# Performance work log

Measured on AMD Instinct MI355X. Metric: run time of the kernel, lower is better.

Reference implementation:

```python
import jax, jax.numpy as jnp
import numpy as np

B, LC, LP = 8, 1024, 512
D, H, F, V, NL = 512, 8, 2048, 70, 4
MAXLEN = 2048
HD = D // H
EPS = 1e-5


def setup_inputs() -> dict:
    key = jax.random.key(0)
    ks = iter(jax.random.split(key, 64))
    s = lambda *sh: jax.random.normal(next(ks), sh, jnp.float32) * 0.02
    inp = {}
    inp['cds'] = jax.random.randint(next(ks), (B, LC), 0, V)
    inp['enc_prot'] = jax.random.normal(next(ks), (B, LP, D), jnp.float32)
    causal = jnp.tril(jnp.ones((LC, LC), jnp.int32))
    inp['cds_mask'] = jnp.broadcast_to(causal[None, None], (B, 1, LC, LC))
    inp['prot_mask'] = jnp.ones((B, 1, 1, LP), jnp.int32)
    inp['tok_emb'] = s(V, D)
    inp['pos_emb'] = s(MAXLEN, D)
    for p in ['sa', 'ca']:
        for m in ['q', 'k', 'v', 'o']:
            inp[f'{p}_w{m}'] = s(NL, D, D)
            inp[f'{p}_b{m}'] = jnp.zeros((NL, D), jnp.float32)
    inp['ff_w1'] = s(NL, D, F)
    inp['ff_b1'] = jnp.zeros((NL, F), jnp.float32)
    inp['ff_w2'] = s(NL, F, D)
    inp['ff_b2'] = jnp.zeros((NL, D), jnp.float32)
    for i in [1, 2, 3]:
        inp[f'ln{i}_g'] = jnp.ones((NL, D), jnp.float32)
        inp[f'ln{i}_b'] = jnp.zeros((NL, D), jnp.float32)
    inp['fc_out_w'] = s(D, V)
    inp['fc_out_b'] = jnp.zeros((V,), jnp.float32)
    return inp


def layernorm(x, g, b):
    mu = jnp.mean(x, -1, keepdims=True)
    var = jnp.var(x, -1, keepdims=True)
    return (x - mu) * jax.lax.rsqrt(var + EPS) * g + b


def mha(q_in, k_in, v_in, wq, bq, wk, bk, wv, bv, wo, bo, mask):
    b, lq, _ = q_in.shape
    lk = k_in.shape[1]
    q = (q_in @ wq + bq).reshape(b, lq, H, HD).transpose(0, 2, 1, 3)
    k = (k_in @ wk + bk).reshape(b, lk, H, HD).transpose(0, 2, 1, 3)
    v = (v_in @ wv + bv).reshape(b, lk, H, HD).transpose(0, 2, 1, 3)
    scores = jnp.einsum('bhqd,bhkd->bhqk', q, k) / jnp.sqrt(jnp.float32(HD))
    scores = jnp.where(mask == 0, -jnp.inf, scores)
    attn = jax.nn.softmax(scores, axis=-1)
    out = jnp.einsum('bhqk,bhkd->bhqd', attn, v)
    out = out.transpose(0, 2, 1, 3).reshape(b, lq, D)
    return out @ wo + bo, attn


def reference(cds, enc_prot, cds_mask, prot_mask, tok_emb, pos_emb,
              sa_wq, sa_bq, sa_wk, sa_bk, sa_wv, sa_bv, sa_wo, sa_bo,
              ca_wq, ca_bq, ca_wk, ca_bk, ca_wv, ca_bv, ca_wo, ca_bo,
              ff_w1, ff_b1, ff_w2, ff_b2,
              ln1_g, ln1_b, ln2_g, ln2_b, ln3_g, ln3_b,
              fc_out_w, fc_out_b):
    lc = cds.shape[1]
    x = tok_emb[cds] * jnp.sqrt(jnp.float32(D)) + pos_emb[:lc][None]
    attn = None
    for i in range(NL):
        sa, _ = mha(x, x, x, sa_wq[i], sa_bq[i], sa_wk[i], sa_bk[i],
                    sa_wv[i], sa_bv[i], sa_wo[i], sa_bo[i], cds_mask)
        x = layernorm(x + sa, ln1_g[i], ln1_b[i])
        ca, attn = mha(x, enc_prot, enc_prot, ca_wq[i], ca_bq[i], ca_wk[i], ca_bk[i],
                       ca_wv[i], ca_bv[i], ca_wo[i], ca_bo[i], prot_mask)
        x = layernorm(x + ca, ln2_g[i], ln2_b[i])
        ff = jax.nn.relu(x @ ff_w1[i] + ff_b1[i]) @ ff_w2[i] + ff_b2[i]
        x = layernorm(x + ff, ln3_g[i], ln3_b[i])
    logits = x @ fc_out_w + fc_out_b
    return logits, attn
```

## Files before the change

kernel.cpp:

```cpp
#include <hip/hip_runtime.h>

typedef __attribute__((ext_vector_type(8))) short bf16x8;
typedef __attribute__((ext_vector_type(4))) short bf16x4;
typedef __attribute__((ext_vector_type(2))) short bf16x2;
typedef __attribute__((ext_vector_type(4))) float f32x4;

#define D_MODEL 512
#define N_HEADS 8
#define HEAD_DIM 64
#define SEQ_C 1024
#define SEQ_P 512
#define BATCH 8
#define FFDIM 2048
#define VOCAB 70
#define NLAYER 4
#define MQ (BATCH*SEQ_C)
#define MKV (BATCH*SEQ_P)
#define KSTR 72
#define SCALE2 0.18033688011112043f

__device__ __forceinline__ short f2bs(float f) {
  union { float f; unsigned u; } v; v.f = f;
  unsigned r = (v.u + 0x7FFFu + ((v.u >> 16) & 1u)) >> 16;
  return (short)r;
}

__device__ __forceinline__ float bs2f(short s) {
  union { float f; unsigned u; } v;
  v.u = ((unsigned)(unsigned short)s) << 16;
  return v.f;
}

__device__ __forceinline__ void gl_lds16(const void* g, void* l) {
  __builtin_amdgcn_global_load_lds(
      (const __attribute__((address_space(1))) void*)g,
      (__attribute__((address_space(3))) void*)l, 16, 0, 0);
}

__global__ __launch_bounds__(256)
void embed_kernel(const int* __restrict__ cds, const float* __restrict__ tok,
                  const float* __restrict__ pos, short* __restrict__ xb) {
  int idx = (blockIdx.x * 256 + threadIdx.x) * 4;
  int row = idx >> 9, c = idx & 511;
  int l = row & (SEQ_C - 1);
  int t = cds[row];
  float4 tv = *(const float4*)(tok + (size_t)t * D_MODEL + c);
  float4 pv = *(const float4*)(pos + (size_t)l * D_MODEL + c);
  bf16x4 o;
  o[0] = f2bs(tv.x * 22.627416997969522f + pv.x);
  o[1] = f2bs(tv.y * 22.627416997969522f + pv.y);
  o[2] = f2bs(tv.z * 22.627416997969522f + pv.z);
  o[3] = f2bs(tv.w * 22.627416997969522f + pv.w);
  *(bf16x4*)(xb + idx) = o;
}

__global__ __launch_bounds__(256)
void cvtf2b_kernel(const float* __restrict__ in, short* __restrict__ out) {
  int i = (blockIdx.x * 256 + threadIdx.x) * 4;
  float4 v = *(const float4*)(in + i);
  bf16x4 o;
  o[0] = f2bs(v.x); o[1] = f2bs(v.y); o[2] = f2bs(v.z); o[3] = f2bs(v.w);
  *(bf16x4*)(out + i) = o;
}

struct WtArgs {
  const float* src[8];
  short* dst[8];
  size_t ldz[8];
  int row_off[8];
};

__global__ __launch_bounds__(256)
void wtrans8_kernel(WtArgs a) {
  __shared__ float T[32][33];
  int z = blockIdx.z;
  int job = z >> 2, layer = z & 3;
  const float* W = a.src[job] + (size_t)layer * D_MODEL * D_MODEL;
  short* Wt = a.dst[job] + (size_t)layer * a.ldz[job];
  int row_off = a.row_off[job];
  int n0 = blockIdx.x * 32, k0 = blockIdx.y * 32;
  int r = threadIdx.x >> 3, c4 = (threadIdx.x & 7) * 4;
  float4 v = *(const float4*)(W + (size_t)(k0 + r) * D_MODEL + n0 + c4);
  T[c4 + 0][r] = v.x; T[c4 + 1][r] = v.y; T[c4 + 2][r] = v.z; T[c4 + 3][r] = v.w;
  __syncthreads();
  bf16x4 o;
  o[0] = f2bs(T[r][c4 + 0]); o[1] = f2bs(T[r][c4 + 1]);
  o[2] = f2bs(T[r][c4 + 2]); o[3] = f2bs(T[r][c4 + 3]);
  *(bf16x4*)&Wt[(size_t)(row_off + n0 + r) * D_MODEL + k0 + c4] = o;
}

__global__ __launch_bounds__(256)
void wtrans_kernel(const float* __restrict__ W, short* __restrict__ Wt,
                   int K, int N, size_t dst_ldz) {
  __shared__ float T[32][33];
  size_t lo_s = (size_t)blockIdx.z * K * N;
  size_t lo_d = (size_t)blockIdx.z * dst_ldz;
  int n0 = blockIdx.x * 32, k0 = blockIdx.y * 32;
  int r = threadIdx.x >> 3, c4 = (threadIdx.x & 7) * 4;
  float4 v = *(const float4*)(W + lo_s + (size_t)(k0 + r) * N + n0 + c4);
  T[c4 + 0][r] = v.x; T[c4 + 1][r] = v.y; T[c4 + 2][r] = v.z; T[c4 + 3][r] = v.w;
  __syncthreads();
  bf16x4 o;
  o[0] = f2bs(T[r][c4 + 0]); o[1] = f2bs(T[r][c4 + 1]);
  o[2] = f2bs(T[r][c4 + 2]); o[3] = f2bs(T[r][c4 + 3]);
  *(bf16x4*)&Wt[lo_d + (size_t)(n0 + r) * K + k0 + c4] = o;
}

__global__ __launch_bounds__(256)
void logits_wt_kernel(const float* __restrict__ w, short* __restrict__ wt) {
  int idx = blockIdx.x * 256 + threadIdx.x;
  int r = idx >> 9, c = idx & 511;
  wt[idx] = (r < VOCAB) ? f2bs(w[c * VOCAB + r]) : (short)0;
}

template<int ACT, int OMODE, int MT, int KSPLIT = 0>
__global__ __launch_bounds__(256)
void gemm_mfma(const short* __restrict__ Ab, const short* __restrict__ Wt,
               const float* __restrict__ b0, const float* __restrict__ b1,
               const float* __restrict__ b2,
               float* __restrict__ Cf, float* __restrict__ Cf2,
               short* __restrict__ Cb,
               int N, int K, int ldc, size_t segstride) {
  constexpr int MREP = MT / 32;
  __shared__ __align__(16) short As[2][MT * 32];
  __shared__ __align__(16) short Bs[2][4096];
  int tid = threadIdx.x, lane = tid & 63, w = tid >> 6;
  int quad = lane >> 4, ln = lane & 15;
  int row0 = blockIdx.x * MT, col0 = blockIdx.y * 128;
  int kz = KSPLIT ? (int)blockIdx.z : 0;
  int Keff = KSPLIT ? (K >> 1) : K;
  int koff = kz * Keff;
  int q0 = tid, q1 = tid + 256;
  const short* a0 = Ab + (size_t)(row0 + (q0 >> 2)) * K + koff + (q0 & 3) * 8;
  const short* a1 = Ab + (size_t)(row0 + (q1 >> 2)) * K + koff + (q1 & 3) * 8;
  const short* w0 = Wt + (size_t)(col0 + (q0 >> 2)) * K + koff + (q0 & 3) * 8;
  const short* w1 = Wt + (size_t)(col0 + (q1 >> 2)) * K + koff + (q1 & 3) * 8;
  int wr = (w >> 1) * (MT / 2), wc = (w & 1) * 64;
  f32x4 acc[MREP][4];
  #pragma unroll
  for (int mb = 0; mb < MREP; mb++)
    #pragma unroll
    for (int nb = 0; nb < 4; nb++) acc[mb][nb] = (f32x4){0.f, 0.f, 0.f, 0.f};

  int nt = Keff >> 5;
#define STG(ko, buf) do { \
    gl_lds16(a0 + (ko), &As[buf][w * 512]); \
    if (MT == 128) gl_lds16(a1 + (ko), &As[buf][MT * 16 + w * 512]); \
    gl_lds16(w0 + (ko), &Bs[buf][w * 512]); \
    gl_lds16(w1 + (ko), &Bs[buf][2048 + w * 512]); } while (0)

  STG(0, 0);
  __syncthreads();
  for (int t = 0; t < nt; t++) {
    int cur = t & 1;
    if (t + 1 < nt) STG((t + 1) << 5, cur ^ 1);
    bf16x8 af[MREP], bfr[4];
    #pragma unroll
    for (int i = 0; i < MREP; i++)
      af[i] = *(const bf16x8*)&As[cur][(wr + i * 16 + ln) * 32 + quad * 8];
    #pragma unroll
    for (int i = 0; i < 4; i++)
      bfr[i] = *(const bf16x8*)&Bs[cur][(wc + i * 16 + ln) * 32 + quad * 8];
    #pragma unroll
    for (int mb = 0; mb < MREP; mb++)
      #pragma unroll
      for (int nb = 0; nb < 4; nb++)
        acc[mb][nb] = __builtin_amdgcn_mfma_f32_16x16x32_bf16(
            af[mb], bfr[nb], acc[mb][nb], 0, 0, 0);
    __syncthreads();
  }
#undef STG

  int colb = col0 + wc;
  const float* bp = b0;
  if (OMODE == 2) {
    int seg = colb >> 9;
    bp = (seg == 0) ? b0 : (seg == 1) ? b1 : b2;
  }
  float bv[4];
  #pragma unroll
  for (int nb = 0; nb < 4; nb++) {
    int col = colb + nb * 16 + ln;
    if (KSPLIT && kz)    bv[nb] = 0.f;
    else if (OMODE == 3) bv[nb] = (col < ldc) ? bp[col] : 0.f;
    else if (OMODE == 2) bv[nb] = bp[col & 511];
    else                 bv[nb] = bp[col];
  }
  float* Co = (KSPLIT && kz) ? Cf2 : Cf;
  size_t segoff = (OMODE == 2) ? (size_t)(colb >> 9) * segstride : 0;
  #pragma unroll
  for (int mb = 0; mb < MREP; mb++)
    #pragma unroll
    for (int i = 0; i < 4; i++) {
      size_t r = (size_t)(row0 + wr + mb * 16 + quad * 4 + i);
      #pragma unroll
      for (int nb = 0; nb < 4; nb++) {
        int col = colb + nb * 16 + ln;
        float v = acc[mb][nb][i] + bv[nb];
        if (ACT) v = fmaxf(v, 0.f);
        if (OMODE == 0)      Co[r * ldc + col] = v;
        else if (OMODE == 1) Cb[r * ldc + col] = f2bs(v);
        else if (OMODE == 2) Cb[segoff + r * 512 + (col & 511)] = f2bs(v);
        else if (col < ldc)  Co[r * ldc + col] = v;
      }
    }
}

__global__ __launch_bounds__(256)
void gemm_mega(const short* __restrict__ A0, const short* __restrict__ W0,
               const float* __restrict__ bq, const float* __restrict__ bk,
               const float* __restrict__ bv0, short* __restrict__ out0,
               const short* __restrict__ A1, const short* __restrict__ W1,
               const float* __restrict__ bk2, const float* __restrict__ bv2,
               short* __restrict__ out1) {
  __shared__ __align__(16) short As[2][4096];
  __shared__ __align__(16) short Bs[2][4096];
  const int K = 512;
  int bid = blockIdx.x;
  int job = bid >= 768;
  const short* Ab; const short* Wt; int row0, col0;
  if (!job) { Ab = A0; Wt = W0; row0 = (bid & 63) << 7; col0 = (bid >> 6) << 7; }
  else { int b2 = bid - 768; Ab = A1; Wt = W1; row0 = (b2 & 31) << 7; col0 = (b2 >> 5) << 7; }
  int tid = threadIdx.x, lane = tid & 63, w = tid >> 6;
  int quad = lane >> 4, ln = lane & 15;
  int q0 = tid, q1 = tid + 256;
  const short* a0 = Ab + (size_t)(row0 + (q0 >> 2)) * K + (q0 & 3) * 8;
  const short* a1 = Ab + (size_t)(row0 + (q1 >> 2)) * K + (q1 & 3) * 8;
  const short* w0 = Wt + (size_t)(col0 + (q0 >> 2)) * K + (q0 & 3) * 8;
  const short* w1 = Wt + (size_t)(col0 + (q1 >> 2)) * K + (q1 & 3) * 8;
  int wr = (w >> 1) * 64, wc = (w & 1) * 64;
  f32x4 acc[4][4];
  #pragma unroll
  for (int mb = 0; mb < 4; mb++)
    #pragma unroll
    for (int nb = 0; nb < 4; nb++) acc[mb][nb] = (f32x4){0.f, 0.f, 0.f, 0.f};

#define STG(ko, buf) do { \
    gl_lds16(a0 + (ko), &As[buf][w * 512]); \
    gl_lds16(a1 + (ko), &As[buf][2048 + w * 512]); \
    gl_lds16(w0 + (ko), &Bs[buf][w * 512]); \
    gl_lds16(w1 + (ko), &Bs[buf][2048 + w * 512]); } while (0)

  STG(0, 0);
  __syncthreads();
  for (int t = 0; t < 16; t++) {
    int cur = t & 1;
    if (t + 1 < 16) STG((t + 1) << 5, cur ^ 1);
    bf16x8 af[4], bfr[4];
    #pragma unroll
    for (int i = 0; i < 4; i++) {
      af[i]  = *(const bf16x8*)&As[cur][(wr + i * 16 + ln) * 32 + quad * 8];
      bfr[i] = *(const bf16x8*)&Bs[cur][(wc + i * 16 + ln) * 32 + quad * 8];
    }
    #pragma unroll
    for (int mb = 0; mb < 4; mb++)
      #pragma unroll
      for (int nb = 0; nb < 4; nb++)
        acc[mb][nb] = __builtin_amdgcn_mfma_f32_16x16x32_bf16(
            af[mb], bfr[nb], acc[mb][nb], 0, 0, 0);
    __syncthreads();
  }
#undef STG

  int colb = col0 + wc;
  int seg = colb >> 9;
  const float* bp = job ? (seg ? bv2 : bk2)
                        : (seg == 0 ? bq : seg == 1 ? bk : bv0);
  short* ob = job ? (out1 + (size_t)seg * ((size_t)MKV * D_MODEL))
                  : (out0 + (size_t)seg * ((size_t)MQ * D_MODEL));
  float bvv[4];
  #pragma unroll
  for (int nb = 0; nb < 4; nb++) bvv[nb] = bp[(colb + nb * 16 + ln) & 511];
  #pragma unroll
  for (int mb = 0; mb < 4; mb++)
    #pragma unroll
    for (int i = 0; i < 4; i++) {
      size_t r = (size_t)(row0 + wr + mb * 16 + quad * 4 + i);
      #pragma unroll
      for (int nb = 0; nb < 4; nb++) {
        int col = colb + nb * 16 + ln;
        ob[r * 512 + (col & 511)] = f2bs(acc[mb][nb][i] + bvv[nb]);
      }
    }
}

template<bool CAUSAL, bool SAVE_ML>
__global__ __launch_bounds__(512)
void flash_mfma(const short* __restrict__ Q, const short* __restrict__ K,
                const short* __restrict__ V, short* __restrict__ O,
                float* __restrict__ m_out, float* __restrict__ l_out,
                int LQ, int LK) {
  __shared__ short Ks[2][64 * KSTR];
  __shared__ short Vt[2][64 * KSTR];
  __shared__ short Ps[8 * 16 * KSTR];
  int qt = CAUSAL ? ((int)gridDim.x - 1 - (int)blockIdx.x) : (int)blockIdx.x;
  int bh = blockIdx.y;
  int b = bh >> 3, h = bh & 7;
  int tid = threadIdx.x, lane = tid & 63, w = tid >> 6;
  int quad = lane >> 4, ln = lane & 15;

  const short* qp = Q + (size_t)(b * LQ + qt * 128 + w * 16 + ln) * D_MODEL + h * HEAD_DIM;
  bf16x8 qf[2];
  qf[0] = *(const bf16x8*)(qp + quad * 8);
  qf[1] = *(const bf16x8*)(qp + 32 + quad * 8);

  int qrow = qt * 128 + w * 16 + ln;
  float m_q = -__builtin_inff(), l_q = 0.f;
  f32x4 o_acc[4];
  #pragma unroll
  for (int nb = 0; nb < 4; nb++) o_acc[nb] = (f32x4){0.f, 0.f, 0.f, 0.f};

  const short* Kb = K + (size_t)(b * LK) * D_MODEL + h * HEAD_DIM;
  const short* Vb = V + (size_t)(b * LK) * D_MODEL + h * HEAD_DIM;
  int sr = tid >> 3, sc = (tid & 7) * 8;
  int br4 = (tid >> 4) * 4, bc4 = (tid & 15) * 4;
  bool vst = tid < 256;

  bf16x8 kr;
  bf16x4 vr0, vr1, vr2, vr3;

#define LOADKV(KT) do { \
    kr = *(const bf16x8*)(Kb + (size_t)((KT) * 64 + sr) * D_MODEL + sc); \
    if (vst) { \
      const short* vg_ = Vb + (size_t)((KT) * 64 + br4) * D_MODEL + bc4; \
      vr0 = *(const bf16x4*)(vg_); \
      vr1 = *(const bf16x4*)(vg_ + D_MODEL); \
      vr2 = *(const bf16x4*)(vg_ + 2 * D_MODEL); \
      vr3 = *(const bf16x4*)(vg_ + 3 * D_MODEL); } } while (0)

#define STORKV(BUF) do { \
    *(bf16x8*)&Ks[BUF][sr * KSTR + sc] = kr; \
    if (vst) { \
      _Pragma("unroll") \
      for (int jj = 0; jj < 4; jj++) { \
        bf16x4 t_; \
        t_[0] = vr0[jj]; t_[1] = vr1[jj]; t_[2] = vr2[jj]; t_[3] = vr3[jj]; \
        *(bf16x4*)&Vt[BUF][(bc4 + jj) * KSTR + br4] = t_; } } } while (0)

  int nkt = CAUSAL ? (2 * qt + 2) : (LK >> 6);
  LOADKV(0);
  STORKV(0);
  if (nkt > 1) LOADKV(1);
  __syncthreads();

  for (int kt = 0; kt < nkt; kt++) {
    int cur = kt & 1;
    if (kt + 1 < nkt) {
      STORKV(cur ^ 1);
      if (kt + 2 < nkt) LOADKV(kt + 2);
    }

    f32x4 st[4];
    __builtin_amdgcn_s_setprio(1);
    #pragma unroll
    for (int nb = 0; nb < 4; nb++) {
      st[nb] = (f32x4){0.f, 0.f, 0.f, 0.f};
      bf16x8 kf0 = *(const bf16x8*)&Ks[cur][(nb * 16 + ln) * KSTR + quad * 8];
      bf16x8 kf1 = *(const bf16x8*)&Ks[cur][(nb * 16 + ln) * KSTR + 32 + quad * 8];
      st[nb] = __builtin_amdgcn_mfma_f32_16x16x32_bf16(kf0, qf[0], st[nb], 0, 0, 0);
      st[nb] = __builtin_amdgcn_mfma_f32_16x16x32_bf16(kf1, qf[1], st[nb], 0, 0, 0);
    }
    __builtin_amdgcn_s_setprio(0);

    float sv[4][4];
    float mt = -__builtin_inff();
    if (CAUSAL && (kt * 64 + 63 > qt * 128 + w * 16)) {
      #pragma unroll
      for (int nb = 0; nb < 4; nb++)
        #pragma unroll
        for (int i = 0; i < 4; i++) {
          float v = st[nb][i] * SCALE2;
          if ((kt * 64 + nb * 16 + quad * 4 + i) > qrow) v = -__builtin_inff();
          sv[nb][i] = v;
          mt = fmaxf(mt, v);
        }
    } else {
      #pragma unroll
      for (int nb = 0; nb < 4; nb++)
        #pragma unroll
        for (int i = 0; i < 4; i++) {
          float v = st[nb][i] * SCALE2;
          sv[nb][i] = v;
          mt = fmaxf(mt, v);
        }
    }
    mt = fmaxf(mt, __shfl_xor(mt, 16));
    mt = fmaxf(mt, __shfl_xor(mt, 32));
    bool skip = __all(mt <= m_q + 8.0f) != 0;
    float mnew = skip ? m_q : fmaxf(m_q, mt);
    if (!skip) {
      float alpha = __builtin_amdgcn_exp2f(m_q - mnew);
      l_q *= alpha;
      #pragma unroll
      for (int i = 0; i < 4; i++) {
        float ai = __shfl(alpha, ((lane >> 4) << 2) + i);
        #pragma unroll
        for (int nb = 0; nb < 4; nb++) o_acc[nb][i] *= ai;
      }
    }
    m_q = mnew;

    float rs = 0.f;
    unsigned pu[4][2];
    #pragma unroll
    for (int nb = 0; nb < 4; nb++) {
      float p0 = __builtin_amdgcn_exp2f(sv[nb][0] - mnew);
      float p1 = __builtin_amdgcn_exp2f(sv[nb][1] - mnew);
      float p2 = __builtin_amdgcn_exp2f(sv[nb][2] - mnew);
      float p3 = __builtin_amdgcn_exp2f(sv[nb][3] - mnew);
      rs += (p0 + p1) + (p2 + p3);
      asm("v_cvt_pk_bf16_f32 %0, %1, %2" : "=v"(pu[nb][0]) : "v"(p0), "v"(p1));
      asm("v_cvt_pk_bf16_f32 %0, %1, %2" : "=v"(pu[nb][1]) : "v"(p2), "v"(p3));
    }
    rs += __shfl_xor(rs, 16);
    rs += __shfl_xor(rs, 32);
    l_q += rs;

    #pragma unroll
    for (int nb = 0; nb < 4; nb++) {
      union { unsigned u[2]; bf16x4 v; } uu;
      uu.u[0] = pu[nb][0]; uu.u[1] = pu[nb][1];
      *(bf16x4*)&Ps[w * 16 * KSTR + ln * KSTR + nb * 16 + quad * 4] = uu.v;
    }

    __builtin_amdgcn_s_setprio(1);
    #pragma unroll
    for (int kb = 0; kb < 2; kb++) {
      bf16x8 pf = *(const bf16x8*)&Ps[w * 16 * KSTR + ln * KSTR + kb * 32 + quad * 8];
      #pragma unroll
      for (int nb = 0; nb < 4; nb++) {
        bf16x8 vf = *(const bf16x8*)&Vt[cur][(nb * 16 + ln) * KSTR + kb * 32 + quad * 8];
        o_acc[nb] = __builtin_amdgcn_mfma_f32_16x16x32_bf16(pf, vf, o_acc[nb], 0, 0, 0);
      }
    }
    __builtin_amdgcn_s_setprio(0);
    __syncthreads();
  }
#undef LOADKV
#undef STORKV

  short* Ob = O + (size_t)(b * LQ + qt * 128 + w * 16 + quad * 4) * D_MODEL + h * HEAD_DIM;
  #pragma unroll
  for (int i = 0; i < 4; i++) {
    float li = __shfl(l_q, ((lane >> 4) << 2) + i);
    float inv = 1.f / li;
    #pragma unroll
    for (int nb = 0; nb < 4; nb++)
      Ob[(size_t)i * D_MODEL + nb * 16 + ln] = f2bs(o_acc[nb][i] * inv);
  }
  if (SAVE_ML && lane < 16) {
    int r = bh * LQ + qt * 128 + w * 16 + lane;
    m_out[r] = m_q;
    l_out[r] = l_q;
  }
}

__global__ __launch_bounds__(256)
void attn_prob_mfma(const short* __restrict__ Q, const short* __restrict__ K,
                    const float* __restrict__ m_in, const float* __restrict__ l_in,
                    float* __restrict__ out) {
  __shared__ short Ks[64 * KSTR];
  int qt = blockIdx.x, bh = blockIdx.y;
  int b = bh >> 3, h = bh & 7;
  int tid = threadIdx.x, lane = tid & 63, w = tid >> 6;
  int quad = lane >> 4, ln = lane & 15;
  const short* qp = Q + (size_t)(b * SEQ_C + qt * 64 + w * 16 + ln) * D_MODEL + h * HEAD_DIM;
  bf16x8 qf[2];
  qf[0] = *(const bf16x8*)(qp + quad * 8);
  qf[1] = *(const bf16x8*)(qp + 32 + quad * 8);
  float m_r[4], il[4];
  #pragma unroll
  for (int i = 0; i < 4; i++) {
    int r = bh * SEQ_C + qt * 64 + w * 16 + quad * 4 + i;
    m_r[i] = m_in[r]; il[i] = 1.f / l_in[r];
  }
  const short* Kb = K + (size_t)(b * SEQ_P) * D_MODEL + h * HEAD_DIM;
  int sr = tid >> 2, sc = (tid & 3) * 16;
  bf16x8 krA, krB;
  {
    const short* kg = Kb + (size_t)sr * D_MODEL + sc;
    krA = *(const bf16x8*)kg; krB = *(const bf16x8*)(kg + 8);
  }
  for (int kt = 0; kt < (SEQ_P >> 6); kt++) {
    __syncthreads();
    *(bf16x8*)&Ks[sr * KSTR + sc]     = krA;
    *(bf16x8*)&Ks[sr * KSTR + sc + 8] = krB;
    if (kt + 1 < (SEQ_P >> 6)) {
      const short* kg = Kb + (size_t)((kt + 1) * 64 + sr) * D_MODEL + sc;
      krA = *(const bf16x8*)kg; krB = *(const bf16x8*)(kg + 8);
    }
    __syncthreads();
    #pragma unroll
    for (int nb = 0; nb < 4; nb++) {
      f32x4 s = (f32x4){0.f, 0.f, 0.f, 0.f};
      bf16x8 kf0 = *(const bf16x8*)&Ks[(nb * 16 + ln) * KSTR + quad * 8];
      bf16x8 kf1 = *(const bf16x8*)&Ks[(nb * 16 + ln) * KSTR + 32 + quad * 8];
      s = __builtin_amdgcn_mfma_f32_16x16x32_bf16(qf[0], kf0, s, 0, 0, 0);
      s = __builtin_amdgcn_mfma_f32_16x16x32_bf16(qf[1], kf1, s, 0, 0, 0);
      #pragma unroll
      for (int i = 0; i < 4; i++) {
        size_t off = ((size_t)bh * SEQ_C + qt * 64 + w * 16 + quad * 4 + i) * SEQ_P
                   + kt * 64 + nb * 16 + ln;
        out[off] = __builtin_amdgcn_exp2f(s[i] * SCALE2 - m_r[i]) * il[i];
      }
    }
  }
}

template<int MODE>
__global__ __launch_bounds__(256)
void add_ln_kernel(short* __restrict__ xb, const short* __restrict__ ybf,
                   const float* __restrict__ yf, const float* __restrict__ y2f,
                   const float* __restrict__ g, const float* __restrict__ b) {
  int row = blockIdx.x * 4 + (threadIdx.x >> 6);
  int lane = threadIdx.x & 63;
  int c0 = lane * 8;
  short* xr = xb + (size_t)row * D_MODEL;
  float v[8]; float s = 0.f, sq = 0.f;
  bf16x8 xv = *(const bf16x8*)(xr + c0);
  if (MODE == 0) {
    bf16x8 yv = *(const bf16x8*)(ybf + (size_t)row * D_MODEL + c0);
    #pragma unroll
    for (int i = 0; i < 8; i++) {
      float t = bs2f(xv[i]) + bs2f(yv[i]);
      v[i] = t; s += t; sq += t * t;
    }
  } else {
    const float* yr = yf + (size_t)row * D_MODEL + c0;
    const float* y2r = y2f + (size_t)row * D_MODEL + c0;
    float4 a0 = *(const float4*)(yr);
    float4 a1 = *(const float4*)(yr + 4);
    float4 c0v = *(const float4*)(y2r);
    float4 c1v = *(const float4*)(y2r + 4);
    float ya[8] = {a0.x + c0v.x, a0.y + c0v.y, a0.z + c0v.z, a0.w + c0v.w,
                   a1.x + c1v.x, a1.y + c1v.y, a1.z + c1v.z, a1.w + c1v.w};
    #pragma unroll
    for (int i = 0; i < 8; i++) {
      float t = bs2f(xv[i]) + ya[i];
      v[i] = t; s += t; sq += t * t;
    }
  }
  #pragma unroll
  for (int m = 1; m < 64; m <<= 1) { s += __shfl_xor(s, m); sq += __shfl_xor(sq, m); }
  float mu = s * (1.0f / 512.0f);
  float var = sq * (1.0f / 512.0f) - mu * mu;
  float rstd = rsqrtf(var + 1e-5f);
  float4 g0 = *(const float4*)(g + c0);
  float4 g1 = *(const float4*)(g + c0 + 4);
  float4 b0 = *(const float4*)(b + c0);
  float4 b1 = *(const float4*)(b + c0 + 4);
  float ga[8] = {g0.x, g0.y, g0.z, g0.w, g1.x, g1.y, g1.z, g1.w};
  float ba[8] = {b0.x, b0.y, b0.z, b0.w, b1.x, b1.y, b1.z, b1.w};
  bf16x8 o;
  #pragma unroll
  for (int i = 0; i < 8; i++)
    o[i] = f2bs((v[i] - mu) * rstd * ga[i] + ba[i]);
  *(bf16x8*)(xr + c0) = o;
}

extern "C" void kernel_launch(void* const* d_in, const int* in_sizes, int n_in,
                              void* d_out, int out_size, void* d_ws, size_t ws_size,
                              hipStream_t stream) {
  (void)in_sizes; (void)n_in; (void)out_size; (void)ws_size;
  const int*   cds      = (const int*)d_in[0];
  const float* enc_prot = (const float*)d_in[1];
  const float* tok_emb  = (const float*)d_in[4];
  const float* pos_emb  = (const float*)d_in[5];
  const float* sa_wq = (const float*)d_in[6];  const float* sa_bq = (const float*)d_in[7];
  const float* sa_wk = (const float*)d_in[8];  const float* sa_bk = (const float*)d_in[9];
  const float* sa_wv = (const float*)d_in[10]; const float* sa_bv = (const float*)d_in[11];
  const float* sa_wo = (const float*)d_in[12]; const float* sa_bo = (const float*)d_in[13];
  const float* ca_wq = (const float*)d_in[14]; const float* ca_bq = (const float*)d_in[15];
  const float* ca_wk = (const float*)d_in[16]; const float* ca_bk = (const float*)d_in[17];
  const float* ca_wv = (const float*)d_in[18]; const float* ca_bv = (const float*)d_in[19];
  const float* ca_wo = (const float*)d_in[20]; const float* ca_bo = (const float*)d_in[21];
  const float* ff_w1 = (const float*)d_in[22]; const float* ff_b1 = (const float*)d_in[23];
  const float* ff_w2 = (const float*)d_in[24]; const float* ff_b2 = (const float*)d_in[25];
  const float* ln1_g = (const float*)d_in[26]; const float* ln1_b = (const float*)d_in[27];
  const float* ln2_g = (const float*)d_in[28]; const float* ln2_b = (const float*)d_in[29];
  const float* ln3_g = (const float*)d_in[30]; const float* ln3_b = (const float*)d_in[31];
  const float* fcw   = (const float*)d_in[32]; const float* fcb   = (const float*)d_in[33];

  float* y    = (float*)d_ws;
  float* mbuf = y + (size_t)MQ * D_MODEL;
  float* lbuf = mbuf + (size_t)BATCH * N_HEADS * SEQ_C;
  short* xb   = (short*)(lbuf + (size_t)BATCH * N_HEADS * SEQ_C);
  short* yb   = xb + (size_t)MQ * D_MODEL;
  short* qb   = yb + (size_t)MQ * D_MODEL;
  short* kb   = qb + (size_t)MQ * D_MODEL;
  short* vb   = kb + (size_t)MQ * D_MODEL;
  short* ctxb = vb + (size_t)MQ * D_MODEL;
  short* hb   = qb;
  short* encb = ctxb + (size_t)MQ * D_MODEL;
  short* ckb  = encb + (size_t)MKV * D_MODEL;
  short* cvb  = ckb + (size_t)MKV * D_MODEL;
  short* wtb  = cvb + (size_t)MKV * D_MODEL;
  short* wts  = wtb + (size_t)128 * D_MODEL;
  const size_t WSZ = (size_t)NLAYER * D_MODEL * D_MODEL;
  short* w_saqkv = wts;
  short* w_sao   = w_saqkv + 3 * WSZ;
  short* w_caq   = w_sao + WSZ;
  short* w_cakv  = w_caq + WSZ;
  short* w_cao   = w_cakv + 2 * WSZ;
  short* w_ff1   = w_cao + WSZ;
  short* w_ff2   = w_ff1 + (size_t)NLAYER * D_MODEL * FFDIM;
  float* y2   = (float*)(w_ff2 + (size_t)NLAYER * D_MODEL * FFDIM);

  float* logits = (float*)d_out;
  float* attn   = logits + (size_t)MQ * VOCAB;

  const size_t L1536 = (size_t)1536 * 512, L1024 = (size_t)1024 * 512, L512 = (size_t)512 * 512;

  embed_kernel<<<MQ * D_MODEL / 1024, 256, 0, stream>>>(cds, tok_emb, pos_emb, xb);
  cvtf2b_kernel<<<(size_t)MKV * D_MODEL / 1024, 256, 0, stream>>>(enc_prot, encb);
  logits_wt_kernel<<<128 * D_MODEL / 256, 256, 0, stream>>>(fcw, wtb);
  {
    WtArgs a;
    a.src[0] = sa_wq; a.dst[0] = w_saqkv; a.ldz[0] = L1536; a.row_off[0] = 0;
    a.src[1] = sa_wk; a.dst[1] = w_saqkv; a.ldz[1] = L1536; a.row_off[1] = 512;
    a.src[2] = sa_wv; a.dst[2] = w_saqkv; a.ldz[2] = L1536; a.row_off[2] = 1024;
    a.src[3] = sa_wo; a.dst[3] = w_sao;   a.ldz[3] = L512;  a.row_off[3] = 0;
    a.src[4] = ca_wq; a.dst[4] = w_caq;   a.ldz[4] = L512;  a.row_off[4] = 0;
    a.src[5] = ca_wk; a.dst[5] = w_cakv;  a.ldz[5] = L1024; a.row_off[5] = 0;
    a.src[6] = ca_wv; a.dst[6] = w_cakv;  a.ldz[6] = L1024; a.row_off[6] = 512;
    a.src[7] = ca_wo; a.dst[7] = w_cao;   a.ldz[7] = L512;  a.row_off[7] = 0;
    wtrans8_kernel<<<dim3(16, 16, 8 * NLAYER), 256, 0, stream>>>(a);
  }
  wtrans_kernel<<<dim3(FFDIM / 32, D_MODEL / 32, NLAYER), 256, 0, stream>>>(
      ff_w1, w_ff1, D_MODEL, FFDIM, (size_t)FFDIM * 512);
  wtrans_kernel<<<dim3(D_MODEL / 32, FFDIM / 32, NLAYER), 256, 0, stream>>>(
      ff_w2, w_ff2, FFDIM, D_MODEL, (size_t)512 * FFDIM);

  dim3 gq64(MQ / 64, D_MODEL / 128);
  dim3 gf1(MQ / 128, FFDIM / 128);
  dim3 gff2(MQ / 128, D_MODEL / 128, 2);
  dim3 glg(MQ / 64, 1);
  dim3 ga(SEQ_C / 128, BATCH * N_HEADS);
  dim3 gap(SEQ_C / 64, BATCH * N_HEADS);

  for (int i = 0; i < NLAYER; i++) {
    size_t wo_ = (size_t)i * D_MODEL * D_MODEL, bo_ = (size_t)i * D_MODEL;
    size_t wf_ = (size_t)i * D_MODEL * FFDIM;
    gemm_mega<<<dim3(1024), 256, 0, stream>>>(
        xb, w_saqkv + (size_t)i * L1536, sa_bq + bo_, sa_bk + bo_, sa_bv + bo_, qb,
        encb, w_cakv + (size_t)i * L1024, ca_bk + bo_, ca_bv + bo_, ckb);
    flash_mfma<true,  false><<<ga, 512, 0, stream>>>(qb, kb, vb, ctxb, nullptr, nullptr, SEQ_C, SEQ_C);
    gemm_mfma<0,1,64><<<gq64, 256, 0, stream>>>(ctxb, w_sao + wo_,
        sa_bo + bo_, nullptr, nullptr, nullptr, nullptr, yb, 512, 512, 512, 0);
    add_ln_kernel<0><<<MQ / 4, 256, 0, stream>>>(xb, yb, nullptr, nullptr, ln1_g + bo_, ln1_b + bo_);
    gemm_mfma<0,1,64><<<gq64, 256, 0, stream>>>(xb, w_caq + wo_,
        ca_bq + bo_, nullptr, nullptr, nullptr, nullptr, qb, 512, 512, 512, 0);
    if (i == NLAYER - 1) {
      flash_mfma<false, true><<<ga, 512, 0, stream>>>(qb, ckb, cvb, ctxb, mbuf, lbuf, SEQ_C, SEQ_P);
      attn_prob_mfma<<<gap, 256, 0, stream>>>(qb, ckb, mbuf, lbuf, attn);
    } else {
      flash_mfma<false, false><<<ga, 512, 0, stream>>>(qb, ckb, cvb, ctxb, nullptr, nullptr, SEQ_C, SEQ_P);
    }
    gemm_mfma<0,1,64><<<gq64, 256, 0, stream>>>(ctxb, w_cao + wo_,
        ca_bo + bo_, nullptr, nullptr, nullptr, nullptr, yb, 512, 512, 512, 0);
    add_ln_kernel<0><<<MQ / 4, 256, 0, stream>>>(xb, yb, nullptr, nullptr, ln2_g + bo_, ln2_b + bo_);
    gemm_mfma<1,1,128><<<gf1, 256, 0, stream>>>(xb, w_ff1 + wf_,
        ff_b1 + (size_t)i * FFDIM, nullptr, nullptr, nullptr, nullptr, hb, FFDIM, 512, FFDIM, 0);
    gemm_mfma<0,0,128,1><<<gff2, 256, 0, stream>>>(hb, w_ff2 + wf_,
        ff_b2 + bo_, nullptr, nullptr, y, y2, nullptr, 512, FFDIM, 512, 0);
    add_ln_kernel<1><<<MQ / 4, 256, 0, stream>>>(xb, nullptr, y, y2, ln3_g + bo_, ln3_b + bo_);
  }
  gemm_mfma<0,3,64><<<glg, 256, 0, stream>>>(xb, wtb,
      fcb, nullptr, nullptr, logits, nullptr, nullptr, 128, 512, VOCAB, 0);
}
```

Measured before the change: 1.145 ms.

## Process two 16-row query tiles per wave in flash attention with 256 threads

The flash attention kernel now runs 4 waves of 256 threads per block instead of 8 waves, and each wave handles 32 query rows as two 16-row sub-tiles. Every K and V fragment read from LDS now feeds two MFMAs, which halves LDS fragment traffic per unit of compute. The softmax logic moves into a helper called once per sub-tile, and the K/V staging loads are redistributed across the smaller thread count. The cost is higher register pressure (two accumulator sets and two score sets) and fewer waves per block to hide latency.

```diff
diff --git a/kernel.cpp b/kernel.cpp
--- a/kernel.cpp
+++ b/kernel.cpp
@@ -284,58 +284,123 @@
     }
 }
 
+template<bool CAUSAL>
+__device__ __forceinline__ void softmax_step(
+    f32x4 st[4], float& m_q, float& l_q, f32x4 o_acc[4],
+    int qrow, bool maybe_masked, int kbase, int quad, int lane,
+    unsigned pu[4][2]) {
+  float sv[4][4];
+  float mt = -__builtin_inff();
+  if (CAUSAL && maybe_masked) {
+    #pragma unroll
+    for (int nb = 0; nb < 4; nb++)
+      #pragma unroll
+      for (int i = 0; i < 4; i++) {
+        float v = st[nb][i] * SCALE2;
+        if ((kbase + nb * 16 + quad * 4 + i) > qrow) v = -__builtin_inff();
+        sv[nb][i] = v;
+        mt = fmaxf(mt, v);
+      }
+  } else {
+    #pragma unroll
+    for (int nb = 0; nb < 4; nb++)
+      #pragma unroll
+      for (int i = 0; i < 4; i++) {
+        float v = st[nb][i] * SCALE2;
+        sv[nb][i] = v;
+        mt = fmaxf(mt, v);
+      }
+  }
+  mt = fmaxf(mt, __shfl_xor(mt, 16));
+  mt = fmaxf(mt, __shfl_xor(mt, 32));
+  bool skip = __all(mt <= m_q + 8.0f) != 0;
+  float mnew = skip ? m_q : fmaxf(m_q, mt);
+  if (!skip) {
+    float alpha = __builtin_amdgcn_exp2f(m_q - mnew);
+    l_q *= alpha;
+    #pragma unroll
+    for (int i = 0; i < 4; i++) {
+      float ai = __shfl(alpha, ((lane >> 4) << 2) + i);
+      #pragma unroll
+      for (int nb = 0; nb < 4; nb++) o_acc[nb][i] *= ai;
+    }
+  }
+  m_q = mnew;
+  float rs = 0.f;
+  #pragma unroll
+  for (int nb = 0; nb < 4; nb++) {
+    float p0 = __builtin_amdgcn_exp2f(sv[nb][0] - mnew);
+    float p1 = __builtin_amdgcn_exp2f(sv[nb][1] - mnew);
+    float p2 = __builtin_amdgcn_exp2f(sv[nb][2] - mnew);
+    float p3 = __builtin_amdgcn_exp2f(sv[nb][3] - mnew);
+    rs += (p0 + p1) + (p2 + p3);
+    asm("v_cvt_pk_bf16_f32 %0, %1, %2" : "=v"(pu[nb][0]) : "v"(p0), "v"(p1));
+    asm("v_cvt_pk_bf16_f32 %0, %1, %2" : "=v"(pu[nb][1]) : "v"(p2), "v"(p3));
+  }
+  rs += __shfl_xor(rs, 16);
+  rs += __shfl_xor(rs, 32);
+  l_q += rs;
+}
+
 template<bool CAUSAL, bool SAVE_ML>
-__global__ __launch_bounds__(512)
+__global__ __launch_bounds__(256)
 void flash_mfma(const short* __restrict__ Q, const short* __restrict__ K,
                 const short* __restrict__ V, short* __restrict__ O,
                 float* __restrict__ m_out, float* __restrict__ l_out,
                 int LQ, int LK) {
   __shared__ short Ks[2][64 * KSTR];
   __shared__ short Vt[2][64 * KSTR];
-  __shared__ short Ps[8 * 16 * KSTR];
+  __shared__ short Ps[4 * 32 * KSTR];
   int qt = CAUSAL ? ((int)gridDim.x - 1 - (int)blockIdx.x) : (int)blockIdx.x;
   int bh = blockIdx.y;
   int b = bh >> 3, h = bh & 7;
   int tid = threadIdx.x, lane = tid & 63, w = tid >> 6;
   int quad = lane >> 4, ln = lane & 15;
 
-  const short* qp = Q + (size_t)(b * LQ + qt * 128 + w * 16 + ln) * D_MODEL + h * HEAD_DIM;
-  bf16x8 qf[2];
-  qf[0] = *(const bf16x8*)(qp + quad * 8);
-  qf[1] = *(const bf16x8*)(qp + 32 + quad * 8);
-
-  int qrow = qt * 128 + w * 16 + ln;
-  float m_q = -__builtin_inff(), l_q = 0.f;
-  f32x4 o_acc[4];
-  #pragma unroll
-  for (int nb = 0; nb < 4; nb++) o_acc[nb] = (f32x4){0.f, 0.f, 0.f, 0.f};
+  const short* qp0 = Q + (size_t)(b * LQ + qt * 128 + w * 32 + ln) * D_MODEL + h * HEAD_DIM;
+  const short* qp1 = qp0 + (size_t)16 * D_MODEL;
+  bf16x8 qf0[2], qf1[2];
+  qf0[0] = *(const bf16x8*)(qp0 + quad * 8);
+  qf0[1] = *(const bf16x8*)(qp0 + 32 + quad * 8);
+  qf1[0] = *(const bf16x8*)(qp1 + quad * 8);
+  qf1[1] = *(const bf16x8*)(qp1 + 32 + quad * 8);
+
+  int qrow0 = qt * 128 + w * 32 + ln;
+  int qrow1 = qrow0 + 16;
+  float m0 = -__builtin_inff(), l0 = 0.f;
+  float m1 = -__builtin_inff(), l1 = 0.f;
+  f32x4 oa0[4], oa1[4];
+  #pragma unroll
+  for (int nb = 0; nb < 4; nb++) {
+    oa0[nb] = (f32x4){0.f, 0.f, 0.f, 0.f};
+    oa1[nb] = (f32x4){0.f, 0.f, 0.f, 0.f};
+  }
 
   const short* Kb = K + (size_t)(b * LK) * D_MODEL + h * HEAD_DIM;
   const short* Vb = V + (size_t)(b * LK) * D_MODEL + h * HEAD_DIM;
-  int sr = tid >> 3, sc = (tid & 7) * 8;
+  int sr = tid >> 2, sc = (tid & 3) * 16;
   int br4 = (tid >> 4) * 4, bc4 = (tid & 15) * 4;
-  bool vst = tid < 256;
-
-  bf16x8 kr;
+
+  bf16x8 krA, krB;
   bf16x4 vr0, vr1, vr2, vr3;
 
 #define LOADKV(KT) do { \
-    kr = *(const bf16x8*)(Kb + (size_t)((KT) * 64 + sr) * D_MODEL + sc); \
-    if (vst) { \
-      const short* vg_ = Vb + (size_t)((KT) * 64 + br4) * D_MODEL + bc4; \
-      vr0 = *(const bf16x4*)(vg_); \
-      vr1 = *(const bf16x4*)(vg_ + D_MODEL); \
-      vr2 = *(const bf16x4*)(vg_ + 2 * D_MODEL); \
-      vr3 = *(const bf16x4*)(vg_ + 3 * D_MODEL); } } while (0)
+    const short* kg_ = Kb + (size_t)((KT) * 64 + sr) * D_MODEL + sc; \
+    krA = *(const bf16x8*)kg_; krB = *(const bf16x8*)(kg_ + 8); \
+    const short* vg_ = Vb + (size_t)((KT) * 64 + br4) * D_MODEL + bc4; \
+    vr0 = *(const bf16x4*)(vg_); \
+    vr1 = *(const bf16x4*)(vg_ + D_MODEL); \
+    vr2 = *(const bf16x4*)(vg_ + 2 * D_MODEL); \
+    vr3 = *(const bf16x4*)(vg_ + 3 * D_MODEL); } while (0)
 
 #define STORKV(BUF) do { \
-    *(bf16x8*)&Ks[BUF][sr * KSTR + sc] = kr; \
-    if (vst) { \
-      _Pragma("unroll") \
-      for (int jj = 0; jj < 4; jj++) { \
-        bf16x4 t_; \
-        t_[0] = vr0[jj]; t_[1] = vr1[jj]; t_[2] = vr2[jj]; t_[3] = vr3[jj]; \
-        *(bf16x4*)&Vt[BUF][(bc4 + jj) * KSTR + br4] = t_; } } } while (0)
+    *(bf16x8*)&Ks[BUF][sr * KSTR + sc] = krA; \
+    *(bf16x8*)&Ks[BUF][sr * KSTR + sc + 8] = krB; \
+    _Pragma("unroll") \
+    for (int jj = 0; jj < 4; jj++) { \
+      bf16x4 t_; \
+      t_[0] = vr0[jj]; t_[1] = vr1[jj]; t_[2] = vr2[jj]; t_[3] = vr3[jj]; \
+      *(bf16x4*)&Vt[BUF][(bc4 + jj) * KSTR + br4] = t_; } } while (0)
 
   int nkt = CAUSAL ? (2 * qt + 2) : (LK >> 6);
   LOADKV(0);
@@ -350,87 +415,47 @@
       if (kt + 2 < nkt) LOADKV(kt + 2);
     }
 
-    f32x4 st[4];
+    f32x4 st0[4], st1[4];
     __builtin_amdgcn_s_setprio(1);
     #pragma unroll
     for (int nb = 0; nb < 4; nb++) {
-      st[nb] = (f32x4){0.f, 0.f, 0.f, 0.f};
+      st0[nb] = (f32x4){0.f, 0.f, 0.f, 0.f};
+      st1[nb] = (f32x4){0.f, 0.f, 0.f, 0.f};
       bf16x8 kf0 = *(const bf16x8*)&Ks[cur][(nb * 16 + ln) * KSTR + quad * 8];
       bf16x8 kf1 = *(const bf16x8*)&Ks[cur][(nb * 16 + ln) * KSTR + 32 + quad * 8];
-      st[nb] = __builtin_amdgcn_mfma_f32_16x16x32_bf16(kf0, qf[0], st[nb], 0, 0, 0);
-      st[nb] = __builtin_amdgcn_mfma_f32_16x16x32_bf16(kf1, qf[1], st[nb], 0, 0, 0);
+      st0[nb] = __builtin_amdgcn_mfma_f32_16x16x32_bf16(kf0, qf0[0], st0[nb], 0, 0, 0);
+      st1[nb] = __builtin_amdgcn_mfma_f32_16x16x32_bf16(kf0, qf1[0], st1[nb], 0, 0, 0);
+      st0[nb] = __builtin_amdgcn_mfma_f32_16x16x32_bf16(kf1, qf0[1], st0[nb], 0, 0, 0);
+      st1[nb] = __builtin_amdgcn_mfma_f32_16x16x32_bf16(kf1, qf1[1], st1[nb], 0, 0, 0);
     }
     __builtin_amdgcn_s_setprio(0);
 
-    float sv[4][4];
-    float mt = -__builtin_inff();
-    if (CAUSAL && (kt * 64 + 63 > qt * 128 + w * 16)) {
-      #pragma unroll
-      for (int nb = 0; nb < 4; nb++)
-        #pragma unroll
-        for (int i = 0; i < 4; i++) {
-          float v = st[nb][i] * SCALE2;
-          if ((kt * 64 + nb * 16 + quad * 4 + i) > qrow) v = -__builtin_inff();
-          sv[nb][i] = v;
-          mt = fmaxf(mt, v);
-        }
-    } else {
-      #pragma unroll
-      for (int nb = 0; nb < 4; nb++)
-        #pragma unroll
-        for (int i = 0; i < 4; i++) {
-          float v = st[nb][i] * SCALE2;
-          sv[nb][i] = v;
-          mt = fmaxf(mt, v);
-        }
-    }
-    mt = fmaxf(mt, __shfl_xor(mt, 16));
-    mt = fmaxf(mt, __shfl_xor(mt, 32));
-    bool skip = __all(mt <= m_q + 8.0f) != 0;
-    float mnew = skip ? m_q : fmaxf(m_q, mt);
-    if (!skip) {
-      float alpha = __builtin_amdgcn_exp2f(m_q - mnew);
-      l_q *= alpha;
-      #pragma unroll
-      for (int i = 0; i < 4; i++) {
-        float ai = __shfl(alpha, ((lane >> 4) << 2) + i);
-        #pragma unroll
-        for (int nb = 0; nb < 4; nb++) o_acc[nb][i] *= ai;
-      }
-    }
-    m_q = mnew;
-
-    float rs = 0.f;
-    unsigned pu[4][2];
+    int kbase = kt * 64;
+    unsigned pu0[4][2], pu1[4][2];
+    bool mm0 = (kbase + 63) > (qt * 128 + w * 32);
+    bool mm1 = (kbase + 63) > (qt * 128 + w * 32 + 16);
+    softmax_step<CAUSAL>(st0, m0, l0, oa0, qrow0, mm0, kbase, quad, lane, pu0);
+    softmax_step<CAUSAL>(st1, m1, l1, oa1, qrow1, mm1, kbase, quad, lane, pu1);
+
     #pragma unroll
     for (int nb = 0; nb < 4; nb++) {
-      float p0 = __builtin_amdgcn_exp2f(sv[nb][0] - mnew);
-      float p1 = __builtin_amdgcn_exp2f(sv[nb][1] - mnew);
-      float p2 = __builtin_amdgcn_exp2f(sv[nb][2] - mnew);
-      float p3 = __builtin_amdgcn_exp2f(sv[nb][3] - mnew);
-      rs += (p0 + p1) + (p2 + p3);
-      asm("v_cvt_pk_bf16_f32 %0, %1, %2" : "=v"(pu[nb][0]) : "v"(p0), "v"(p1));
-      asm("v_cvt_pk_bf16_f32 %0, %1, %2" : "=v"(pu[nb][1]) : "v"(p2), "v"(p3));
-    }
-    rs += __shfl_xor(rs, 16);
-    rs += __shfl_xor(rs, 32);
-    l_q += rs;
-
-    #pragma unroll
-    for (int nb = 0; nb < 4; nb++) {
-      union { unsigned u[2]; bf16x4 v; } uu;
-      uu.u[0] = pu[nb][0]; uu.u[1] = pu[nb][1];
-      *(bf16x4*)&Ps[w * 16 * KSTR + ln * KSTR + nb * 16 + quad * 4] = uu.v;
+      union { unsigned u[2]; bf16x4 v; } a, bq;
+      a.u[0] = pu0[nb][0]; a.u[1] = pu0[nb][1];
+      bq.u[0] = pu1[nb][0]; bq.u[1] = pu1[nb][1];
+      *(bf16x4*)&Ps[(w * 32 + ln) * KSTR + nb * 16 + quad * 4] = a.v;
+      *(bf16x4*)&Ps[(w * 32 + 16 + ln) * KSTR + nb * 16 + quad * 4] = bq.v;
     }
 
     __builtin_amdgcn_s_setprio(1);
     #pragma unroll
     for (int kb = 0; kb < 2; kb++) {
-      bf16x8 pf = *(const bf16x8*)&Ps[w * 16 * KSTR + ln * KSTR + kb * 32 + quad * 8];
+      bf16x8 pf0 = *(const bf16x8*)&Ps[(w * 32 + ln) * KSTR + kb * 32 + quad * 8];
+      bf16x8 pf1 = *(const bf16x8*)&Ps[(w * 32 + 16 + ln) * KSTR + kb * 32 + quad * 8];
       #pragma unroll
       for (int nb = 0; nb < 4; nb++) {
         bf16x8 vf = *(const bf16x8*)&Vt[cur][(nb * 16 + ln) * KSTR + kb * 32 + quad * 8];
-        o_acc[nb] = __builtin_amdgcn_mfma_f32_16x16x32_bf16(pf, vf, o_acc[nb], 0, 0, 0);
+        oa0[nb] = __builtin_amdgcn_mfma_f32_16x16x32_bf16(pf0, vf, oa0[nb], 0, 0, 0);
+        oa1[nb] = __builtin_amdgcn_mfma_f32_16x16x32_bf16(pf1, vf, oa1[nb], 0, 0, 0);
       }
     }
     __builtin_amdgcn_s_setprio(0);
@@ -439,19 +464,23 @@
 #undef LOADKV
 #undef STORKV
 
-  short* Ob = O + (size_t)(b * LQ + qt * 128 + w * 16 + quad * 4) * D_MODEL + h * HEAD_DIM;
+  short* Ob0 = O + (size_t)(b * LQ + qt * 128 + w * 32 + quad * 4) * D_MODEL + h * HEAD_DIM;
+  short* Ob1 = Ob0 + (size_t)16 * D_MODEL;
   #pragma unroll
   for (int i = 0; i < 4; i++) {
-    float li = __shfl(l_q, ((lane >> 4) << 2) + i);
-    float inv = 1.f / li;
-    #pragma unroll
-    for (int nb = 0; nb < 4; nb++)
-      Ob[(size_t)i * D_MODEL + nb * 16 + ln] = f2bs(o_acc[nb][i] * inv);
+    float li0 = __shfl(l0, ((lane >> 4) << 2) + i);
+    float li1 = __shfl(l1, ((lane >> 4) << 2) + i);
+    float iv0 = 1.f / li0, iv1 = 1.f / li1;
+    #pragma unroll
+    for (int nb = 0; nb < 4; nb++) {
+      Ob0[(size_t)i * D_MODEL + nb * 16 + ln] = f2bs(oa0[nb][i] * iv0);
+      Ob1[(size_t)i * D_MODEL + nb * 16 + ln] = f2bs(oa1[nb][i] * iv1);
+    }
   }
   if (SAVE_ML && lane < 16) {
-    int r = bh * LQ + qt * 128 + w * 16 + lane;
-    m_out[r] = m_q;
-    l_out[r] = l_q;
+    int r0 = bh * LQ + qt * 128 + w * 32 + lane;
+    m_out[r0] = m0; l_out[r0] = l0;
+    m_out[r0 + 16] = m1; l_out[r0 + 16] = l1;
   }
 }
 
@@ -644,17 +673,17 @@
     gemm_mega<<<dim3(1024), 256, 0, stream>>>(
         xb, w_saqkv + (size_t)i * L1536, sa_bq + bo_, sa_bk + bo_, sa_bv + bo_, qb,
         encb, w_cakv + (size_t)i * L1024, ca_bk + bo_, ca_bv + bo_, ckb);
-    flash_mfma<true,  false><<<ga, 512, 0, stream>>>(qb, kb, vb, ctxb, nullptr, nullptr, SEQ_C, SEQ_C);
+    flash_mfma<true,  false><<<ga, 256, 0, stream>>>(qb, kb, vb, ctxb, nullptr, nullptr, SEQ_C, SEQ_C);
     gemm_mfma<0,1,64><<<gq64, 256, 0, stream>>>(ctxb, w_sao + wo_,
         sa_bo + bo_, nullptr, nullptr, nullptr, nullptr, yb, 512, 512, 512, 0);
     add_ln_kernel<0><<<MQ / 4, 256, 0, stream>>>(xb, yb, nullptr, nullptr, ln1_g + bo_, ln1_b + bo_);
     gemm_mfma<0,1,64><<<gq64, 256, 0, stream>>>(xb, w_caq + wo_,
         ca_bq + bo_, nullptr, nullptr, nullptr, nullptr, qb, 512, 512, 512, 0);
     if (i == NLAYER - 1) {
-      flash_mfma<false, true><<<ga, 512, 0, stream>>>(qb, ckb, cvb, ctxb, mbuf, lbuf, SEQ_C, SEQ_P);
+      flash_mfma<false, true><<<ga, 256, 0, stream>>>(qb, ckb, cvb, ctxb, mbuf, lbuf, SEQ_C, SEQ_P);
       attn_prob_mfma<<<gap, 256, 0, stream>>>(qb, ckb, mbuf, lbuf, attn);
     } else {
-      flash_mfma<false, false><<<ga, 512, 0, stream>>>(qb, ckb, cvb, ctxb, nullptr, nullptr, SEQ_C, SEQ_P);
+      flash_mfma<false, false><<<ga, 256, 0, stream>>>(qb, ckb, cvb, ctxb, nullptr, nullptr, SEQ_C, SEQ_P);
     }
     gemm_mfma<0,1,64><<<gq64, 256, 0, stream>>>(ctxb, w_cao + wo_,
         ca_bo + bo_, nullptr, nullptr, nullptr, nullptr, yb, 512, 512, 512, 0);
```

After: 1.174 ms. +2.5%, slower.
